# Kernel optimization log

Hardware: AMD Instinct MI355X
Metric: run time of the kernel (lower is better)

The kernel has to match this reference:

```python
import jax, jax.numpy as jnp
import numpy as np

N_NODES = 200000  # graph size
D = 128           # feature dim == out_size
N1 = 81920        # layer-1 node set size
B = 8192          # batch size
K = 10            # num_sample neighbors


def setup_inputs() -> dict:
    key = jax.random.key(0)
    k = jax.random.split(key, 7)
    raw_features = jax.random.normal(k[0], (N_NODES, D), dtype=jnp.float32)
    # xavier-like scale for weights [out, 2*in]
    W1 = jax.random.normal(k[1], (D, 2 * D), dtype=jnp.float32) * (1.0 / np.sqrt(2 * D))
    W2 = jax.random.normal(k[2], (D, 2 * D), dtype=jnp.float32) * (1.0 / np.sqrt(2 * D))
    layer1_nodes = jax.random.randint(k[3], (N1,), 0, N_NODES)
    neigh0_idx = jax.random.randint(k[4], (N1, K), 0, N_NODES)
    map_batch = jax.random.randint(k[5], (B,), 0, N1)
    neigh1_idx = jax.random.randint(k[6], (B, K), 0, N1)
    return {
        "raw_features": raw_features,
        "W1": W1,
        "W2": W2,
        "layer1_nodes": layer1_nodes,
        "neigh0_idx": neigh0_idx,
        "map_batch": map_batch,
        "neigh1_idx": neigh1_idx,
    }


def _sage_layer(self_feats, agg_feats, W):
    # combined = cat([self, agg], dim=1); relu(W @ combined.T).T == relu(combined @ W.T)
    combined = jnp.concatenate([self_feats, agg_feats], axis=1)
    return jax.nn.relu(combined @ W.T)


def reference(raw_features, W1, W2, layer1_nodes, neigh0_idx, map_batch, neigh1_idx):
    # Layer 1: aggregate raw features over K sampled neighbors (MEAN), gcn=False
    agg0 = jnp.mean(raw_features[neigh0_idx], axis=1)        # [N1, D]
    self0 = raw_features[layer1_nodes]                        # [N1, D]
    h1 = _sage_layer(self0, agg0, W1)                         # [N1, D]
    # Layer 2: aggregate layer-1 embeddings for the batch nodes
    agg1 = jnp.mean(h1[neigh1_idx], axis=1)                   # [B, D]
    self1 = h1[map_batch]                                     # [B, D]
    h2 = _sage_layer(self1, agg1, W2)                         # [B, D]
    return h2
```

## Files before the change

### kernel.cpp

```cpp
#include <hip/hip_runtime.h>
#include <stdint.h>

#define D 128
#define K_NEI 10
#define TILE_M 64

typedef __bf16 bf16x8 __attribute__((ext_vector_type(8)));
typedef float f32x4 __attribute__((ext_vector_type(4)));

__device__ __forceinline__ uint32_t f2bf(float f) {
    union { float f; uint32_t u; } v; v.f = f;
    uint32_t u = v.u;
    return (u + 0x7FFFu + ((u >> 16) & 1u)) >> 16;
}
__device__ __forceinline__ float bf2f(uint32_t h) {
    union { uint32_t u; float f; } v; v.u = h << 16; return v.f;
}
__device__ __forceinline__ uint32_t pack2(float a, float b) {
    return f2bf(a) | (f2bf(b) << 16);
}
__device__ __forceinline__ bf16x8 u4_as_bf16x8(uint4 u) {
    union { uint4 u; bf16x8 b; } v; v.u = u; return v.b;
}

__global__ void convert_W2(const float* __restrict__ Wa, const float* __restrict__ Wb_in,
                           uint16_t* __restrict__ Oa, uint16_t* __restrict__ Ob)
{
    const float* W = (blockIdx.x < 16) ? Wa : Wb_in;
    uint16_t*    O = (blockIdx.x < 16) ? Oa : Ob;
    int t = (blockIdx.x & 15) * 256 + threadIdx.x;
    int c = t >> 4, j = t & 15;
    const float* src = W + (size_t)(c & 127) * 256 + (c >> 7) * 128 + j * 8;
    f32x4 a = *(const f32x4*)src;
    f32x4 b = *(const f32x4*)(src + 4);
    uint4 o;
    o.x = pack2(a[0], a[1]); o.y = pack2(a[2], a[3]);
    o.z = pack2(b[0], b[1]); o.w = pack2(b[2], b[3]);
    *(uint4*)(O + (size_t)c * 128 + j * 8) = o;
}

template <bool A_F32>
__global__ __launch_bounds__(256)
void gemm_ws(const void* __restrict__ Asrc_,
             const uint16_t* __restrict__ Wb,
             uint16_t* __restrict__ P, int M)
{
    __shared__ __align__(16) uint16_t Wlds[256 * 128];

    const int tid  = threadIdx.x;
    const int wave = tid >> 6;
    const int lane = tid & 63;
    const int r16  = lane & 15;
    const int q    = lane >> 4;

    #pragma unroll
    for (int it = 0; it < 16; ++it) {
        int t = it * 256 + tid;
        int j = t >> 4, c = t & 15;
        uint4 v = *(const uint4*)(Wb + (size_t)j * 128 + c * 8);
        int cs = c ^ (j & 15);
        *(uint4*)(Wlds + j * 128 + cs * 8) = v;
    }
    __syncthreads();

    const int nTiles = M >> 4;
    const int stride = gridDim.x * 4;
    int tile = blockIdx.x * 4 + wave;
    if (tile >= nTiles) return;

    f32x4 preF[8];  uint4 preB[4];

    if (A_F32) {
        const float* row = (const float*)Asrc_ + (size_t)(tile * 16 + r16) * D + q * 8;
        #pragma unroll
        for (int ks = 0; ks < 4; ++ks) {
            preF[2 * ks]     = *(const f32x4*)(row + ks * 32);
            preF[2 * ks + 1] = *(const f32x4*)(row + ks * 32 + 4);
        }
    } else {
        const uint16_t* row = (const uint16_t*)Asrc_ + (size_t)(tile * 16 + r16) * D + q * 8;
        #pragma unroll
        for (int ks = 0; ks < 4; ++ks)
            preB[ks] = *(const uint4*)(row + ks * 32);
    }

    while (tile < nTiles) {
        const int nxt = tile + stride;

        bf16x8 a[4];
        if (A_F32) {
            #pragma unroll
            for (int ks = 0; ks < 4; ++ks) {
                uint4 u;
                u.x = pack2(preF[2*ks][0],   preF[2*ks][1]);
                u.y = pack2(preF[2*ks][2],   preF[2*ks][3]);
                u.z = pack2(preF[2*ks+1][0], preF[2*ks+1][1]);
                u.w = pack2(preF[2*ks+1][2], preF[2*ks+1][3]);
                a[ks] = u4_as_bf16x8(u);
            }
        } else {
            #pragma unroll
            for (int ks = 0; ks < 4; ++ks) a[ks] = u4_as_bf16x8(preB[ks]);
        }

        if (nxt < nTiles) {
            if (A_F32) {
                const float* row = (const float*)Asrc_ + (size_t)(nxt * 16 + r16) * D + q * 8;
                #pragma unroll
                for (int ks = 0; ks < 4; ++ks) {
                    preF[2 * ks]     = *(const f32x4*)(row + ks * 32);
                    preF[2 * ks + 1] = *(const f32x4*)(row + ks * 32 + 4);
                }
            } else {
                const uint16_t* row = (const uint16_t*)Asrc_ + (size_t)(nxt * 16 + r16) * D + q * 8;
                #pragma unroll
                for (int ks = 0; ks < 4; ++ks)
                    preB[ks] = *(const uint4*)(row + ks * 32);
            }
        }

        f32x4 acc[2][8];
        #pragma unroll
        for (int h = 0; h < 2; ++h)
            #pragma unroll
            for (int nt = 0; nt < 8; ++nt) acc[h][nt] = (f32x4){0.f, 0.f, 0.f, 0.f};

        #pragma unroll
        for (int h = 0; h < 2; ++h)
            #pragma unroll
            for (int ks = 0; ks < 4; ++ks) {
                const int cidx = ks * 4 + q;
                #pragma unroll
                for (int nt = 0; nt < 8; ++nt) {
                    const int jj = h * 128 + nt * 16 + r16;
                    bf16x8 b = *(const bf16x8*)(Wlds + jj * 128 + ((cidx ^ r16) * 8));
                    acc[h][nt] = __builtin_amdgcn_mfma_f32_16x16x32_bf16(a[ks], b, acc[h][nt], 0, 0, 0);
                }
            }

        const int row0 = tile * 16 + q * 4;
        #pragma unroll
        for (int h = 0; h < 2; ++h)
            #pragma unroll
            for (int nt = 0; nt < 8; ++nt) {
                const int col = h * 128 + nt * 16 + r16;
                #pragma unroll
                for (int r = 0; r < 4; ++r)
                    P[(size_t)(row0 + r) * 256 + col] = (uint16_t)f2bf(acc[h][nt][r]);
            }

        tile = nxt;
    }
}

template <bool OUT_F32>
__global__ void combine(const uint16_t* __restrict__ P,
                        const int* __restrict__ self_idx,
                        const int* __restrict__ neigh_idx,
                        void* __restrict__ out_, int M)
{
    const int t = blockIdx.x * 256 + threadIdx.x;
    const int i = t >> 4;
    const int j = t & 15;
    if (i >= M) return;

    uint4 sv = *(const uint4*)(P + (size_t)self_idx[i] * 256 + j * 8);

    const int2* nrow2 = (const int2*)(neigh_idx + (size_t)i * K_NEI);
    int idx[K_NEI];
    #pragma unroll
    for (int k = 0; k < 5; ++k) {
        int2 p = nrow2[k];
        idx[2 * k] = p.x; idx[2 * k + 1] = p.y;
    }

    float s0=0,s1=0,s2=0,s3=0,s4=0,s5=0,s6=0,s7=0;
    #pragma unroll
    for (int k = 0; k < K_NEI; ++k) {
        uint4 v = *(const uint4*)(P + (size_t)idx[k] * 256 + 128 + j * 8);
        s0 += bf2f(v.x & 0xFFFFu); s1 += bf2f(v.x >> 16);
        s2 += bf2f(v.y & 0xFFFFu); s3 += bf2f(v.y >> 16);
        s4 += bf2f(v.z & 0xFFFFu); s5 += bf2f(v.z >> 16);
        s6 += bf2f(v.w & 0xFFFFu); s7 += bf2f(v.w >> 16);
    }
    const float inv = 0.1f;
    float r0 = bf2f(sv.x & 0xFFFFu) + s0 * inv, r1 = bf2f(sv.x >> 16) + s1 * inv;
    float r2 = bf2f(sv.y & 0xFFFFu) + s2 * inv, r3 = bf2f(sv.y >> 16) + s3 * inv;
    float r4 = bf2f(sv.z & 0xFFFFu) + s4 * inv, r5 = bf2f(sv.z >> 16) + s5 * inv;
    float r6 = bf2f(sv.w & 0xFFFFu) + s6 * inv, r7 = bf2f(sv.w >> 16) + s7 * inv;
    r0 = r0 > 0.f ? r0 : 0.f; r1 = r1 > 0.f ? r1 : 0.f;
    r2 = r2 > 0.f ? r2 : 0.f; r3 = r3 > 0.f ? r3 : 0.f;
    r4 = r4 > 0.f ? r4 : 0.f; r5 = r5 > 0.f ? r5 : 0.f;
    r6 = r6 > 0.f ? r6 : 0.f; r7 = r7 > 0.f ? r7 : 0.f;

    if (OUT_F32) {
        float* dst = (float*)out_ + (size_t)i * D + j * 8;
        *(f32x4*)dst       = (f32x4){r0, r1, r2, r3};
        *(f32x4*)(dst + 4) = (f32x4){r4, r5, r6, r7};
    } else {
        uint4 o;
        o.x = pack2(r0, r1); o.y = pack2(r2, r3);
        o.z = pack2(r4, r5); o.w = pack2(r6, r7);
        *(uint4*)((uint16_t*)out_ + (size_t)i * D + j * 8) = o;
    }
}

template <bool FEATS_F32, bool OUT_F32>
__global__ void sage_layer(const void* __restrict__ feats_,
                           const float* __restrict__ W,
                           const int* __restrict__ self_idx,
                           const int* __restrict__ neigh_idx,
                           void* __restrict__ out_)
{
    __shared__ __align__(16) uint16_t Alds[TILE_M * 128];
    __shared__ __align__(16) uint16_t Wlds[128 * 128];

    const int tid  = threadIdx.x;
    const int wave = tid >> 6;
    const int lane = tid & 63;
    const int r16  = lane & 15;
    const int q    = lane >> 4;
    const int G    = blockIdx.x * TILE_M;

    const float*    feats_f = (const float*)feats_;
    const uint16_t* feats_b = (const uint16_t*)feats_;

    f32x4 acc[8];
    #pragma unroll
    for (int nt = 0; nt < 8; ++nt) acc[nt] = (f32x4){0.f, 0.f, 0.f, 0.f};

    for (int half = 0; half < 2; ++half) {
        #pragma unroll
        for (int it = 0; it < 8; ++it) {
            int t = it * 256 + tid;
            int j = t >> 4, c = t & 15;
            const float* src = W + (size_t)j * 256 + half * 128 + c * 8;
            f32x4 w0 = *(const f32x4*)(src);
            f32x4 w1 = *(const f32x4*)(src + 4);
            uint4 o;
            o.x = pack2(w0[0], w0[1]); o.y = pack2(w0[2], w0[3]);
            o.z = pack2(w1[0], w1[1]); o.w = pack2(w1[2], w1[3]);
            int cs = c ^ (j & 15);
            *(uint4*)(Wlds + j * 128 + cs * 8) = o;
        }
        if (half == 0) {
            #pragma unroll
            for (int it = 0; it < 4; ++it) {
                int t = it * 256 + tid;
                int n = t >> 4, c = t & 15;
                int node = self_idx[G + n];
                uint4 o;
                if (FEATS_F32) {
                    const float* src = feats_f + (size_t)node * D + c * 8;
                    f32x4 f0 = *(const f32x4*)(src);
                    f32x4 f1 = *(const f32x4*)(src + 4);
                    o.x = pack2(f0[0], f0[1]); o.y = pack2(f0[2], f0[3]);
                    o.z = pack2(f1[0], f1[1]); o.w = pack2(f1[2], f1[3]);
                } else {
                    o = *(const uint4*)(feats_b + (size_t)node * D + c * 8);
                }
                int cs = c ^ (n & 15);
                *(uint4*)(Alds + n * 128 + cs * 8) = o;
            }
        } else {
            #pragma unroll
            for (int it = 0; it < 4; ++it) {
                int t = it * 256 + tid;
                int n = t >> 4, c = t & 15;
                const int* nrow = neigh_idx + (size_t)(G + n) * K_NEI;
                float s0=0,s1=0,s2=0,s3=0,s4=0,s5=0,s6=0,s7=0;
                #pragma unroll
                for (int k = 0; k < K_NEI; ++k) {
                    if (FEATS_F32) {
                        const float* src = feats_f + (size_t)nrow[k] * D + c * 8;
                        f32x4 f0 = *(const f32x4*)(src);
                        f32x4 f1 = *(const f32x4*)(src + 4);
                        s0 += f0[0]; s1 += f0[1]; s2 += f0[2]; s3 += f0[3];
                        s4 += f1[0]; s5 += f1[1]; s6 += f1[2]; s7 += f1[3];
                    } else {
                        uint4 v = *(const uint4*)(feats_b + (size_t)nrow[k] * D + c * 8);
                        s0 += bf2f(v.x & 0xFFFFu); s1 += bf2f(v.x >> 16);
                        s2 += bf2f(v.y & 0xFFFFu); s3 += bf2f(v.y >> 16);
                        s4 += bf2f(v.z & 0xFFFFu); s5 += bf2f(v.z >> 16);
                        s6 += bf2f(v.w & 0xFFFFu); s7 += bf2f(v.w >> 16);
                    }
                }
                const float inv = 0.1f;
                uint4 o;
                o.x = pack2(s0 * inv, s1 * inv);
                o.y = pack2(s2 * inv, s3 * inv);
                o.z = pack2(s4 * inv, s5 * inv);
                o.w = pack2(s6 * inv, s7 * inv);
                int cs = c ^ (n & 15);
                *(uint4*)(Alds + n * 128 + cs * 8) = o;
            }
        }
        __syncthreads();

        #pragma unroll
        for (int ks = 0; ks < 4; ++ks) {
            int cidx = ks * 4 + q;
            bf16x8 a = *(const bf16x8*)(Alds + (wave * 16 + r16) * 128 + ((cidx ^ r16) * 8));
            bf16x8 b[8];
            #pragma unroll
            for (int nt = 0; nt < 8; ++nt) {
                int jj = nt * 16 + r16;
                b[nt] = *(const bf16x8*)(Wlds + jj * 128 + ((cidx ^ r16) * 8));
            }
            #pragma unroll
            for (int nt = 0; nt < 8; ++nt)
                acc[nt] = __builtin_amdgcn_mfma_f32_16x16x32_bf16(a, b[nt], acc[nt], 0, 0, 0);
        }
        __syncthreads();
    }

    const int row_base = G + wave * 16 + q * 4;
    #pragma unroll
    for (int nt = 0; nt < 8; ++nt) {
        int col = nt * 16 + r16;
        #pragma unroll
        for (int r = 0; r < 4; ++r) {
            float v = acc[nt][r];
            v = v > 0.f ? v : 0.f;
            if (OUT_F32) ((float*)out_)[(size_t)(row_base + r) * D + col] = v;
            else ((uint16_t*)out_)[(size_t)(row_base + r) * D + col] = (uint16_t)f2bf(v);
        }
    }
}

extern "C" void kernel_launch(void* const* d_in, const int* in_sizes, int n_in,
                              void* d_out, int out_size, void* d_ws, size_t ws_size,
                              hipStream_t stream) {
    const float* raw = (const float*)d_in[0];
    const float* W1  = (const float*)d_in[1];
    const float* W2  = (const float*)d_in[2];
    const int* layer1_nodes = (const int*)d_in[3];
    const int* neigh0       = (const int*)d_in[4];
    const int* map_batch    = (const int*)d_in[5];
    const int* neigh1       = (const int*)d_in[6];

    const int N_NODES = in_sizes[0] / D;
    const int N1 = in_sizes[3];
    const int B  = in_sizes[5];

    const size_t szP  = (size_t)N_NODES * 256 * 2;
    const size_t szQ  = (size_t)N1 * 256 * 2;
    const size_t szH1 = (size_t)N1 * 128 * 2;
    const size_t szW  = 256 * 128 * 2;
    const size_t needA = (szP > szQ ? szP : szQ) + szH1 + 2 * szW;

    if (ws_size >= needA && (N_NODES % 16) == 0 && (N1 % 16) == 0 && (B % 16) == 0) {
        uint16_t* Pbuf = (uint16_t*)d_ws;
        uint16_t* h1   = (uint16_t*)((char*)d_ws + (szP > szQ ? szP : szQ));
        uint16_t* W1b  = h1 + (size_t)N1 * 128;
        uint16_t* W2b  = W1b + 256 * 128;

        convert_W2<<<32, 256, 0, stream>>>(W1, W2, W1b, W2b);

        int tiles1 = N_NODES >> 4;
        int grid1  = 1024;
        gemm_ws<true ><<<grid1, 256, 0, stream>>>(raw, W1b, Pbuf, N_NODES);

        combine<false><<<(N1 * 16 + 255) / 256, 256, 0, stream>>>(Pbuf, layer1_nodes, neigh0, h1, N1);

        int tiles2 = N1 >> 4;
        int grid2  = (tiles2 + 3) / 4;
        if (grid2 > 1280) grid2 = 1280;
        gemm_ws<false><<<grid2, 256, 0, stream>>>(h1, W2b, Pbuf, N1);

        combine<true ><<<(B * 16 + 255) / 256, 256, 0, stream>>>(Pbuf, map_batch, neigh1, d_out, B);
        return;
    }

    uint16_t* h1 = (uint16_t*)d_ws;
    sage_layer<true,  false><<<N1 / TILE_M, 256, 0, stream>>>(raw, W1, layer1_nodes, neigh0, h1);
    sage_layer<false, true ><<<B  / TILE_M, 256, 0, stream>>>(h1,  W2, map_batch,    neigh1, d_out);
}
```

Measured before the change: 243.2 us.

## Split GEMM output columns across grid y to halve LDS and accumulators

The weight-projection GEMM is split into two blocks per output half (blockIdx.y selects which 128 output columns), so each block stages only half of W in LDS and holds half the accumulators, and launch bounds request 4 blocks per CU. The epilogue now packs two bf16 outputs per 32-bit store using a lane shuffle instead of scattered 16-bit stores. The aim is higher occupancy and wider stores, at the cost of reading each A tile twice, once per column half.

After: 417.5 us. +71.6%, slower.

```diff
diff --git a/kernel.cpp b/kernel.cpp
--- a/kernel.cpp
+++ b/kernel.cpp
@@ -40,24 +40,26 @@
 }
 
 template <bool A_F32>
-__global__ __launch_bounds__(256)
-void gemm_ws(const void* __restrict__ Asrc_,
-             const uint16_t* __restrict__ Wb,
-             uint16_t* __restrict__ P, int M)
+__global__ __launch_bounds__(256, 4)
+void gemm_half(const void* __restrict__ Asrc_,
+               const uint16_t* __restrict__ Wb,
+               uint16_t* __restrict__ P, int M)
 {
-    __shared__ __align__(16) uint16_t Wlds[256 * 128];
+    __shared__ __align__(16) uint16_t Wlds[128 * 128];
 
     const int tid  = threadIdx.x;
     const int wave = tid >> 6;
     const int lane = tid & 63;
     const int r16  = lane & 15;
     const int q    = lane >> 4;
-
-    #pragma unroll
-    for (int it = 0; it < 16; ++it) {
+    const int h    = blockIdx.y;
+
+    const uint16_t* Wsrc = Wb + (size_t)h * 128 * 128;
+    #pragma unroll
+    for (int it = 0; it < 8; ++it) {
         int t = it * 256 + tid;
         int j = t >> 4, c = t & 15;
-        uint4 v = *(const uint4*)(Wb + (size_t)j * 128 + c * 8);
+        uint4 v = *(const uint4*)(Wsrc + (size_t)j * 128 + c * 8);
         int cs = c ^ (j & 15);
         *(uint4*)(Wlds + j * 128 + cs * 8) = v;
     }
@@ -119,35 +121,35 @@
             }
         }
 
-        f32x4 acc[2][8];
-        #pragma unroll
-        for (int h = 0; h < 2; ++h)
-            #pragma unroll
-            for (int nt = 0; nt < 8; ++nt) acc[h][nt] = (f32x4){0.f, 0.f, 0.f, 0.f};
-
-        #pragma unroll
-        for (int h = 0; h < 2; ++h)
-            #pragma unroll
-            for (int ks = 0; ks < 4; ++ks) {
-                const int cidx = ks * 4 + q;
-                #pragma unroll
-                for (int nt = 0; nt < 8; ++nt) {
-                    const int jj = h * 128 + nt * 16 + r16;
-                    bf16x8 b = *(const bf16x8*)(Wlds + jj * 128 + ((cidx ^ r16) * 8));
-                    acc[h][nt] = __builtin_amdgcn_mfma_f32_16x16x32_bf16(a[ks], b, acc[h][nt], 0, 0, 0);
+        f32x4 acc[8];
+        #pragma unroll
+        for (int nt = 0; nt < 8; ++nt) acc[nt] = (f32x4){0.f, 0.f, 0.f, 0.f};
+
+        #pragma unroll
+        for (int ks = 0; ks < 4; ++ks) {
+            const int cidx = ks * 4 + q;
+            #pragma unroll
+            for (int nt = 0; nt < 8; ++nt) {
+                const int jj = nt * 16 + r16;
+                bf16x8 b = *(const bf16x8*)(Wlds + jj * 128 + ((cidx ^ r16) * 8));
+                acc[nt] = __builtin_amdgcn_mfma_f32_16x16x32_bf16(a[ks], b, acc[nt], 0, 0, 0);
+            }
+        }
+
+        const int row0 = tile * 16 + q * 4;
+        const bool evenlane = (r16 & 1) == 0;
+        #pragma unroll
+        for (int nt = 0; nt < 8; ++nt) {
+            const int colE = h * 128 + nt * 16 + (r16 & ~1);
+            #pragma unroll
+            for (int r = 0; r < 4; ++r) {
+                float v = acc[nt][r];
+                float w = __shfl_xor(v, 1);
+                if (evenlane) {
+                    *(uint32_t*)(P + (size_t)(row0 + r) * 256 + colE) = pack2(v, w);
                 }
             }
-
-        const int row0 = tile * 16 + q * 4;
-        #pragma unroll
-        for (int h = 0; h < 2; ++h)
-            #pragma unroll
-            for (int nt = 0; nt < 8; ++nt) {
-                const int col = h * 128 + nt * 16 + r16;
-                #pragma unroll
-                for (int r = 0; r < 4; ++r)
-                    P[(size_t)(row0 + r) * 256 + col] = (uint16_t)f2bf(acc[h][nt][r]);
-            }
+        }
 
         tile = nxt;
     }
@@ -357,16 +359,11 @@
 
         convert_W2<<<32, 256, 0, stream>>>(W1, W2, W1b, W2b);
 
-        int tiles1 = N_NODES >> 4;
-        int grid1  = 1024;
-        gemm_ws<true ><<<grid1, 256, 0, stream>>>(raw, W1b, Pbuf, N_NODES);
+        gemm_half<true ><<<dim3(640, 2), 256, 0, stream>>>(raw, W1b, Pbuf, N_NODES);
 
         combine<false><<<(N1 * 16 + 255) / 256, 256, 0, stream>>>(Pbuf, layer1_nodes, neigh0, h1, N1);
 
-        int tiles2 = N1 >> 4;
-        int grid2  = (tiles2 + 3) / 4;
-        if (grid2 > 1280) grid2 = 1280;
-        gemm_ws<false><<<grid2, 256, 0, stream>>>(h1, W2b, Pbuf, N1);
+        gemm_half<false><<<dim3(320, 2), 256, 0, stream>>>(h1, W2b, Pbuf, N1);
 
         combine<true ><<<(B * 16 + 255) / 256, 256, 0, stream>>>(Pbuf, map_batch, neigh1, d_out, B);
         return;
```

## Fuse weight bf16 conversion into GEMM and stage half of W in LDS

Applied to the files above, without the earlier changes.

Drops the separate weight-conversion kernel. Each GEMM block now converts fp32 W to bf16 itself and writes it into a 32KB LDS buffer, one 128-column half at a time. Blocks process 64-row tiles with four waves and no longer prefetch the next A tile. The aim is to save one kernel launch and the workspace for bf16 weights, and to raise occupancy with the smaller LDS footprint. The cost is that every tile re-reads and re-converts all of W from global/L2, adds extra barriers, and loses the A-load overlap.

Result: slower. 287.8 us (+18.3%).

```diff
diff --git a/kernel.cpp b/kernel.cpp
--- a/kernel.cpp
+++ b/kernel.cpp
@@ -23,29 +23,13 @@
     union { uint4 u; bf16x8 b; } v; v.u = u; return v.b;
 }
 
-__global__ void convert_W2(const float* __restrict__ Wa, const float* __restrict__ Wb_in,
-                           uint16_t* __restrict__ Oa, uint16_t* __restrict__ Ob)
-{
-    const float* W = (blockIdx.x < 16) ? Wa : Wb_in;
-    uint16_t*    O = (blockIdx.x < 16) ? Oa : Ob;
-    int t = (blockIdx.x & 15) * 256 + threadIdx.x;
-    int c = t >> 4, j = t & 15;
-    const float* src = W + (size_t)(c & 127) * 256 + (c >> 7) * 128 + j * 8;
-    f32x4 a = *(const f32x4*)src;
-    f32x4 b = *(const f32x4*)(src + 4);
-    uint4 o;
-    o.x = pack2(a[0], a[1]); o.y = pack2(a[2], a[3]);
-    o.z = pack2(b[0], b[1]); o.w = pack2(b[2], b[3]);
-    *(uint4*)(O + (size_t)c * 128 + j * 8) = o;
-}
-
 template <bool A_F32>
-__global__ __launch_bounds__(256)
-void gemm_ws(const void* __restrict__ Asrc_,
-             const uint16_t* __restrict__ Wb,
+__global__ __launch_bounds__(256, 4)
+void gemm_rw(const void* __restrict__ Asrc_,
+             const float* __restrict__ W,
              uint16_t* __restrict__ P, int M)
 {
-    __shared__ __align__(16) uint16_t Wlds[256 * 128];
+    __shared__ __align__(16) uint16_t Wlds[128 * 128];
 
     const int tid  = threadIdx.x;
     const int wave = tid >> 6;
@@ -53,70 +37,34 @@
     const int r16  = lane & 15;
     const int q    = lane >> 4;
 
-    #pragma unroll
-    for (int it = 0; it < 16; ++it) {
-        int t = it * 256 + tid;
-        int j = t >> 4, c = t & 15;
-        uint4 v = *(const uint4*)(Wb + (size_t)j * 128 + c * 8);
-        int cs = c ^ (j & 15);
-        *(uint4*)(Wlds + j * 128 + cs * 8) = v;
-    }
-    __syncthreads();
-
-    const int nTiles = M >> 4;
-    const int stride = gridDim.x * 4;
-    int tile = blockIdx.x * 4 + wave;
-    if (tile >= nTiles) return;
-
-    f32x4 preF[8];  uint4 preB[4];
-
-    if (A_F32) {
-        const float* row = (const float*)Asrc_ + (size_t)(tile * 16 + r16) * D + q * 8;
-        #pragma unroll
-        for (int ks = 0; ks < 4; ++ks) {
-            preF[2 * ks]     = *(const f32x4*)(row + ks * 32);
-            preF[2 * ks + 1] = *(const f32x4*)(row + ks * 32 + 4);
-        }
-    } else {
-        const uint16_t* row = (const uint16_t*)Asrc_ + (size_t)(tile * 16 + r16) * D + q * 8;
-        #pragma unroll
-        for (int ks = 0; ks < 4; ++ks)
-            preB[ks] = *(const uint4*)(row + ks * 32);
-    }
-
-    while (tile < nTiles) {
-        const int nxt = tile + stride;
+    const int nTiles = M >> 6;
+    for (int tile = blockIdx.x; tile < nTiles; tile += gridDim.x) {
 
         bf16x8 a[4];
         if (A_F32) {
+            const float* row = (const float*)Asrc_
+                             + (size_t)(tile * 64 + wave * 16 + r16) * D + q * 8;
+            f32x4 raw[8];
+            #pragma unroll
+            for (int ks = 0; ks < 4; ++ks) {
+                raw[2 * ks]     = *(const f32x4*)(row + ks * 32);
+                raw[2 * ks + 1] = *(const f32x4*)(row + ks * 32 + 4);
+            }
             #pragma unroll
             for (int ks = 0; ks < 4; ++ks) {
                 uint4 u;
-                u.x = pack2(preF[2*ks][0],   preF[2*ks][1]);
-                u.y = pack2(preF[2*ks][2],   preF[2*ks][3]);
-                u.z = pack2(preF[2*ks+1][0], preF[2*ks+1][1]);
-                u.w = pack2(preF[2*ks+1][2], preF[2*ks+1][3]);
+                u.x = pack2(raw[2*ks][0],   raw[2*ks][1]);
+                u.y = pack2(raw[2*ks][2],   raw[2*ks][3]);
+                u.z = pack2(raw[2*ks+1][0], raw[2*ks+1][1]);
+                u.w = pack2(raw[2*ks+1][2], raw[2*ks+1][3]);
                 a[ks] = u4_as_bf16x8(u);
             }
         } else {
-            #pragma unroll
-            for (int ks = 0; ks < 4; ++ks) a[ks] = u4_as_bf16x8(preB[ks]);
-        }
-
-        if (nxt < nTiles) {
-            if (A_F32) {
-                const float* row = (const float*)Asrc_ + (size_t)(nxt * 16 + r16) * D + q * 8;
-                #pragma unroll
-                for (int ks = 0; ks < 4; ++ks) {
-                    preF[2 * ks]     = *(const f32x4*)(row + ks * 32);
-                    preF[2 * ks + 1] = *(const f32x4*)(row + ks * 32 + 4);
-                }
-            } else {
-                const uint16_t* row = (const uint16_t*)Asrc_ + (size_t)(nxt * 16 + r16) * D + q * 8;
-                #pragma unroll
-                for (int ks = 0; ks < 4; ++ks)
-                    preB[ks] = *(const uint4*)(row + ks * 32);
-            }
+            const uint16_t* row = (const uint16_t*)Asrc_
+                                + (size_t)(tile * 64 + wave * 16 + r16) * D + q * 8;
+            #pragma unroll
+            for (int ks = 0; ks < 4; ++ks)
+                a[ks] = u4_as_bf16x8(*(const uint4*)(row + ks * 32));
         }
 
         f32x4 acc[2][8];
@@ -126,19 +74,36 @@
             for (int nt = 0; nt < 8; ++nt) acc[h][nt] = (f32x4){0.f, 0.f, 0.f, 0.f};
 
         #pragma unroll
-        for (int h = 0; h < 2; ++h)
+        for (int h = 0; h < 2; ++h) {
+            #pragma unroll
+            for (int it = 0; it < 8; ++it) {
+                int t = it * 256 + tid;
+                int j = t >> 4, c = t & 15;
+                const float* src = W + (size_t)j * 256 + h * 128 + c * 8;
+                f32x4 w0 = *(const f32x4*)(src);
+                f32x4 w1 = *(const f32x4*)(src + 4);
+                uint4 o;
+                o.x = pack2(w0[0], w0[1]); o.y = pack2(w0[2], w0[3]);
+                o.z = pack2(w1[0], w1[1]); o.w = pack2(w1[2], w1[3]);
+                int cs = c ^ (j & 15);
+                *(uint4*)(Wlds + j * 128 + cs * 8) = o;
+            }
+            __syncthreads();
+
             #pragma unroll
             for (int ks = 0; ks < 4; ++ks) {
                 const int cidx = ks * 4 + q;
                 #pragma unroll
                 for (int nt = 0; nt < 8; ++nt) {
-                    const int jj = h * 128 + nt * 16 + r16;
+                    const int jj = nt * 16 + r16;
                     bf16x8 b = *(const bf16x8*)(Wlds + jj * 128 + ((cidx ^ r16) * 8));
                     acc[h][nt] = __builtin_amdgcn_mfma_f32_16x16x32_bf16(a[ks], b, acc[h][nt], 0, 0, 0);
                 }
             }
-
-        const int row0 = tile * 16 + q * 4;
+            __syncthreads();
+        }
+
+        const int row0 = tile * 64 + wave * 16 + q * 4;
         #pragma unroll
         for (int h = 0; h < 2; ++h)
             #pragma unroll
@@ -148,8 +113,6 @@
                 for (int r = 0; r < 4; ++r)
                     P[(size_t)(row0 + r) * 256 + col] = (uint16_t)f2bf(acc[h][nt][r]);
             }
-
-        tile = nxt;
     }
 }
 
@@ -346,27 +309,21 @@
     const size_t szP  = (size_t)N_NODES * 256 * 2;
     const size_t szQ  = (size_t)N1 * 256 * 2;
     const size_t szH1 = (size_t)N1 * 128 * 2;
-    const size_t szW  = 256 * 128 * 2;
-    const size_t needA = (szP > szQ ? szP : szQ) + szH1 + 2 * szW;
-
-    if (ws_size >= needA && (N_NODES % 16) == 0 && (N1 % 16) == 0 && (B % 16) == 0) {
+    const size_t needA = (szP > szQ ? szP : szQ) + szH1;
+
+    if (ws_size >= needA && (N_NODES % 64) == 0 && (N1 % 64) == 0 && (B % 16) == 0) {
         uint16_t* Pbuf = (uint16_t*)d_ws;
         uint16_t* h1   = (uint16_t*)((char*)d_ws + (szP > szQ ? szP : szQ));
-        uint16_t* W1b  = h1 + (size_t)N1 * 128;
-        uint16_t* W2b  = W1b + 256 * 128;
-
-        convert_W2<<<32, 256, 0, stream>>>(W1, W2, W1b, W2b);
-
-        int tiles1 = N_NODES >> 4;
-        int grid1  = 1024;
-        gemm_ws<true ><<<grid1, 256, 0, stream>>>(raw, W1b, Pbuf, N_NODES);
+
+        int tiles1 = N_NODES >> 6;
+        int grid1  = tiles1 < 1280 ? tiles1 : 1280;
+        gemm_rw<true ><<<grid1, 256, 0, stream>>>(raw, W1, Pbuf, N_NODES);
 
         combine<false><<<(N1 * 16 + 255) / 256, 256, 0, stream>>>(Pbuf, layer1_nodes, neigh0, h1, N1);
 
-        int tiles2 = N1 >> 4;
-        int grid2  = (tiles2 + 3) / 4;
-        if (grid2 > 1280) grid2 = 1280;
-        gemm_ws<false><<<grid2, 256, 0, stream>>>(h1, W2b, Pbuf, N1);
+        int tiles2 = N1 >> 6;
+        int grid2  = tiles2 < 1280 ? tiles2 : 1280;
+        gemm_rw<false><<<grid2, 256, 0, stream>>>(h1, W2, Pbuf, N1);
 
         combine<true ><<<(B * 16 + 255) / 256, 256, 0, stream>>>(Pbuf, map_batch, neigh1, d_out, B);
         return;
```
